# Kernel tuning notes

Measured on AMD Instinct MI355X. Metric: run time of the kernel, lower is better.

The kernel has to match this reference:

```python
import jax, jax.numpy as jnp
import numpy as np

N = 40000
E = 200000
D = 32
NUM_BANDS = 3
ORDER = 4
EPS = 1e-8
LN_EPS = 1e-5


def setup_inputs() -> dict:
    key = jax.random.key(0)
    ks = jax.random.split(key, 20)
    h = jax.random.normal(ks[0], (N, D), dtype=jnp.float32)
    Q = jax.random.normal(ks[1], (E, D, D), dtype=jnp.float32) / jnp.sqrt(jnp.float32(D))
    edge_index = jax.random.randint(ks[2], (2, E), 0, N, dtype=jnp.int32)
    coeffs = jnp.ones((NUM_BANDS, ORDER + 1), dtype=jnp.float32) / (ORDER + 1)
    s = 1.0 / np.sqrt(D)
    proj_W = jax.random.uniform(ks[3], (NUM_BANDS, D, D), minval=-s, maxval=s, dtype=jnp.float32)
    proj_b = jax.random.uniform(ks[4], (NUM_BANDS, D), minval=-s, maxval=s, dtype=jnp.float32)
    proj_g = jnp.ones((NUM_BANDS, D), dtype=jnp.float32)
    proj_beta = jnp.zeros((NUM_BANDS, D), dtype=jnp.float32)
    s3 = 1.0 / np.sqrt(NUM_BANDS * D)
    fus_W1 = jax.random.uniform(ks[5], (NUM_BANDS * D, D), minval=-s3, maxval=s3, dtype=jnp.float32)
    fus_b1 = jax.random.uniform(ks[6], (D,), minval=-s3, maxval=s3, dtype=jnp.float32)
    fus_g = jnp.ones((D,), dtype=jnp.float32)
    fus_beta = jnp.zeros((D,), dtype=jnp.float32)
    fus_W2 = jax.random.uniform(ks[7], (D, D), minval=-s, maxval=s, dtype=jnp.float32)
    fus_b2 = jax.random.uniform(ks[8], (D,), minval=-s, maxval=s, dtype=jnp.float32)
    return {"h": h, "Q": Q, "edge_index": edge_index, "coeffs": coeffs,
            "proj_W": proj_W, "proj_b": proj_b, "proj_g": proj_g, "proj_beta": proj_beta,
            "fus_W1": fus_W1, "fus_b1": fus_b1, "fus_g": fus_g, "fus_beta": fus_beta,
            "fus_W2": fus_W2, "fus_b2": fus_b2}


def _layer_norm(x, g, b):
    mu = x.mean(-1, keepdims=True)
    var = x.var(-1, keepdims=True)  # biased, as torch LayerNorm
    return (x - mu) / jnp.sqrt(var + LN_EPS) * g + b


def reference(h, Q, edge_index, coeffs, proj_W, proj_b, proj_g, proj_beta,
              fus_W1, fus_b1, fus_g, fus_beta, fus_W2, fus_b2):
    row, col = edge_index[0], edge_index[1]
    n = h.shape[0]
    ones_e = jnp.ones(row.shape[0], dtype=h.dtype)
    deg = (jax.ops.segment_sum(ones_e, row, num_segments=n)
           + jax.ops.segment_sum(ones_e, col, num_segments=n))  # [N]

    def matvec(x):
        # gather -> per-edge DxD bmm -> scatter_add; diag via degree
        Qh = jnp.einsum('eij,ej->ei', Q, x[col])          # [E, D]
        off = jax.ops.segment_sum(Qh, row, num_segments=n)  # [N, D]
        return deg[:, None] * x - off

    # power iteration for lambda_max (5 iters, fixed key for determinism)
    v = jax.random.normal(jax.random.key(42), h.shape, dtype=h.dtype)
    v = v / jnp.linalg.norm(v)
    lam = jnp.array(1.0, dtype=h.dtype)
    for _ in range(5):
        Lv = matvec(v)
        lam = (v * Lv).sum() / ((v * v).sum() + EPS)
        v = Lv / (jnp.linalg.norm(Lv) + EPS)
    lam = jnp.maximum(lam, 1.0)

    def L_tilde(x):
        return 2.0 / (lam + EPS) * matvec(x) - x

    bands = []
    for b_idx in range(NUM_BANDS):
        w = jax.nn.softmax(coeffs[b_idx])
        T_prev = h
        T_curr = L_tilde(h)
        res = w[0] * T_prev + w[1] * T_curr
        for k in range(2, ORDER + 1):
            T_next = 2.0 * L_tilde(T_curr) - T_prev
            res = res + w[k] * T_next
            T_prev, T_curr = T_curr, T_next
        p = jax.nn.silu(_layer_norm(res @ proj_W[b_idx] + proj_b[b_idx],
                                    proj_g[b_idx], proj_beta[b_idx]))
        bands.append(p)

    cat = jnp.concatenate(bands, axis=-1)  # [N, 3D]
    fused = jax.nn.silu(_layer_norm(cat @ fus_W1 + fus_b1, fus_g, fus_beta)) @ fus_W2 + fus_b2
    return h + fused
```

## Files before the change

kernel.cpp:

```cpp
#include <hip/hip_runtime.h>
#include <hip/hip_fp16.h>
#include <math.h>

#define NN 40000
#define EE 200000
#define DD 32
#define ND (NN * DD)
#define LNEPS 1e-5f

typedef float    fv4 __attribute__((ext_vector_type(4)));
typedef unsigned uv4 __attribute__((ext_vector_type(4)));

#define SLOT_ALPHA 48
#define SCAL_FLOATS (64 + 2048 + 64)

__device__ __forceinline__ void threefry2x32(unsigned k0, unsigned k1,
                                             unsigned x0, unsigned x1,
                                             unsigned& o0, unsigned& o1) {
  const unsigned k2 = k0 ^ k1 ^ 0x1BD11BDAu;
  unsigned v0 = x0 + k0, v1 = x1 + k1;
#define TF_ROUND(r) { v0 += v1; v1 = (v1 << (r)) | (v1 >> (32 - (r))); v1 ^= v0; }
  TF_ROUND(13) TF_ROUND(15) TF_ROUND(26) TF_ROUND(6)
  v0 += k1; v1 += k2 + 1u;
  TF_ROUND(17) TF_ROUND(29) TF_ROUND(16) TF_ROUND(24)
  v0 += k2; v1 += k0 + 2u;
  TF_ROUND(13) TF_ROUND(15) TF_ROUND(26) TF_ROUND(6)
  v0 += k0; v1 += k1 + 3u;
  TF_ROUND(17) TF_ROUND(29) TF_ROUND(16) TF_ROUND(24)
  v0 += k1; v1 += k2 + 4u;
  TF_ROUND(13) TF_ROUND(15) TF_ROUND(26) TF_ROUND(6)
  v0 += k2; v1 += k0 + 5u;
#undef TF_ROUND
  o0 = v0; o1 = v1;
}

__device__ __forceinline__ float wave64_sum(float x) {
  for (int o = 32; o > 0; o >>= 1) x += __shfl_xor(x, o, 64);
  return x;
}
__device__ __forceinline__ float g32_sum(float x) {
  for (int o = 16; o > 0; o >>= 1) x += __shfl_xor(x, o, 32);
  return x;
}

__global__ void k_deg(const int* __restrict__ ei, float* __restrict__ deg,
                      int* __restrict__ hist) {
  int e = blockIdx.x * 256 + threadIdx.x;
  if (e < EE) {
    int r = ei[e];
    atomicAdd(deg + r, 1.0f);
    atomicAdd(deg + ei[EE + e], 1.0f);
    atomicAdd(hist + r, 1);
  }
}

__global__ __launch_bounds__(1024) void k_scan(const int* __restrict__ hist,
                                               int* __restrict__ row_start,
                                               int* __restrict__ cursor) {
  __shared__ int part[1024];
  const int t = threadIdx.x;
  const int base = t * 40;
  int s = 0;
  for (int i = base; i < base + 40 && i < NN; ++i) s += hist[i];
  part[t] = s;
  __syncthreads();
  for (int off = 1; off < 1024; off <<= 1) {
    int v = (t >= off) ? part[t - off] : 0;
    __syncthreads();
    part[t] += v;
    __syncthreads();
  }
  int ex = (t == 0) ? 0 : part[t - 1];
  for (int i = base; i < base + 40 && i < NN; ++i) {
    row_start[i] = ex;
    cursor[i] = ex;
    ex += hist[i];
  }
  if (t == 0) row_start[NN] = EE;
}

__global__ void k_genv(float* __restrict__ v, float* __restrict__ vpre,
                       const float* __restrict__ deg) {
  int i = blockIdx.x * 256 + threadIdx.x;
  unsigned o0, o1;
  threefry2x32(0u, 42u, 0u, (unsigned)i, o0, o1);
  unsigned bits = o1;
  float f = __uint_as_float((bits >> 9) | 0x3f800000u) - 1.0f;
  const float lo = -0.99999994f;
  float u = fmaxf(lo, f * 2.0f + lo);
  float val = 1.41421354f * erfinvf(u);
  v[i] = val;
  if (vpre) vpre[i] = deg[i >> 5] * val;
}

__device__ __forceinline__ int clamp8(float q) {
  int v = (int)rintf(q);
  return v < -127 ? -127 : (v > 127 ? 127 : v);
}
__device__ __forceinline__ unsigned pack4v(fv4 q, float inv) {
  int q0 = clamp8(q.x * inv), q1 = clamp8(q.y * inv),
      q2 = clamp8(q.z * inv), q3 = clamp8(q.w * inv);
  return (q0 & 255) | ((q1 & 255) << 8) | ((q2 & 255) << 16) | ((q3 & 255) << 24);
}
__device__ __forceinline__ void dp4(unsigned u, fv4 xv, float& acc) {
  acc = fmaf((float)(signed char)(u),        xv.x, acc);
  acc = fmaf((float)(signed char)(u >> 8),   xv.y, acc);
  acc = fmaf((float)(signed char)(u >> 16),  xv.z, acc);
  acc = fmaf((float)(signed char)(u >> 24),  xv.w, acc);
}

__global__ __launch_bounds__(256) void k_cvt_mv(const float* __restrict__ x,
                                                const float* __restrict__ Q,
                                                const int* __restrict__ ei,
                                                int* __restrict__ cursor,
                                                char* __restrict__ Qi8,
                                                __half* __restrict__ Qs,
                                                int* __restrict__ cols,
                                                float* __restrict__ out) {
  const int slot = threadIdx.x >> 5;
  const int lane = threadIdx.x & 31;
  const int e = blockIdx.x * 8 + slot;
  const int row = ei[e];
  const int col = ei[EE + e];
  int pos = 0;
  if (lane == 0) pos = atomicAdd(cursor + row, 1);
  pos = __shfl(pos, 0, 32);
  const fv4* __restrict__ x4 = (const fv4*)(x + (size_t)col * DD);
  fv4 xr[8];
#pragma unroll
  for (int k = 0; k < 8; ++k) xr[k] = x4[k];
  const fv4* __restrict__ q4 =
      (const fv4*)(Q + (size_t)e * (DD * DD) + (size_t)lane * DD);
  fv4 qf[8];
#pragma unroll
  for (int k = 0; k < 8; ++k) qf[k] = __builtin_nontemporal_load(q4 + k);
  float acc = 0.0f;
#pragma unroll
  for (int k = 0; k < 8; ++k) {
    acc = fmaf(qf[k].x, xr[k].x, acc);
    acc = fmaf(qf[k].y, xr[k].y, acc);
    acc = fmaf(qf[k].z, xr[k].z, acc);
    acc = fmaf(qf[k].w, xr[k].w, acc);
  }
  float m = 0.0f;
#pragma unroll
  for (int k = 0; k < 8; ++k) {
    m = fmaxf(m, fmaxf(fmaxf(fabsf(qf[k].x), fabsf(qf[k].y)),
                       fmaxf(fabsf(qf[k].z), fabsf(qf[k].w))));
  }
  __half sh = __float2half(m * (1.0f / 127.0f));
  float s = __half2float(sh);
  float inv = (s > 0.0f) ? 1.0f / s : 0.0f;
  uv4 pa, pb;
  pa.x = pack4v(qf[0], inv); pa.y = pack4v(qf[1], inv);
  pa.z = pack4v(qf[2], inv); pa.w = pack4v(qf[3], inv);
  pb.x = pack4v(qf[4], inv); pb.y = pack4v(qf[5], inv);
  pb.z = pack4v(qf[6], inv); pb.w = pack4v(qf[7], inv);
  uv4* __restrict__ qs = (uv4*)(Qi8 + (size_t)pos * (DD * DD) + (size_t)lane * DD);
  qs[0] = pa;
  qs[1] = pb;
  Qs[pos * DD + lane] = sh;
  if (lane == 0) cols[pos] = col;
  atomicAdd(out + (size_t)row * DD + lane, -acc);
}

#define CHUNK 16

__global__ __launch_bounds__(256) void k_gather(const float* __restrict__ x,
                                                const float* __restrict__ xprev,
                                                const char* __restrict__ Qi8,
                                                const __half* __restrict__ Qs,
                                                const int* __restrict__ cols,
                                                const int* __restrict__ row_start,
                                                const float* __restrict__ deg,
                                                const float* __restrict__ scal,
                                                float* __restrict__ dots,
                                                float* __restrict__ out, int mode) {
  __shared__ float lds[4][CHUNK][DD];
  __shared__ float d1[4], d2[4];
  const int wid  = threadIdx.x >> 6;
  const int lane = threadIdx.x & 63;
  const int half = lane >> 5;
  const int d    = lane & 31;
  const int r = blockIdx.x * 4 + wid;
  const int beg = row_start[r];
  const int end = row_start[r + 1];
  const int degree = end - beg;

  const size_t idx = (size_t)r * DD + d;
  const float xi = x[idx];
  const float dv = deg[r];
  const float xp = (mode == 2) ? xprev[idx] : 0.0f;

  float acc = 0.0f;
  for (int chunk = 0; chunk < degree; chunk += CHUNK) {
    const int nchunk = min(CHUNK, degree - chunk);
    int myc = (lane < nchunk) ? cols[beg + chunk + lane] : 0;
    {
      const int el = lane >> 2;
      const int pt = lane & 3;
      if (el < nchunk) {
        const int c = __shfl(myc, el, 64);
        const fv4* __restrict__ xs = (const fv4*)(x + (size_t)c * DD);
        fv4 a = xs[pt * 2];
        fv4 b = xs[pt * 2 + 1];
        fv4* __restrict__ dst = (fv4*)&lds[wid][el][pt * 8];
        dst[0] = a;
        dst[1] = b;
      }
    }
    uv4 a0 = {0,0,0,0}, b0 = {0,0,0,0}, a1 = {0,0,0,0}, b1 = {0,0,0,0};
    float s0 = 0.0f, s1 = 0.0f;
#define LOADQ(PP, A, B, S)                                                    \
    if ((PP) < nchunk) {                                                      \
      const size_t pos = (size_t)(beg + chunk + (PP));                        \
      const uv4* __restrict__ q8 =                                            \
          (const uv4*)(Qi8 + pos * (DD * DD) + (size_t)d * DD);               \
      A = q8[0]; B = q8[1];                                                   \
      S = __half2float(Qs[pos * DD + d]);                                     \
    }
    LOADQ(half, a0, b0, s0)
    LOADQ(2 + half, a1, b1, s1)
    for (int p0 = 0; p0 < nchunk; p0 += 2) {
      uv4 a2 = {0,0,0,0}, b2 = {0,0,0,0};
      float s2 = 0.0f;
      LOADQ(p0 + 4 + half, a2, b2, s2)
      const int p = p0 + half;
      if (p < nchunk) {
        const fv4* __restrict__ xl = (const fv4*)&lds[wid][p][0];
        fv4 xr[8];
#pragma unroll
        for (int k = 0; k < 8; ++k) xr[k] = xl[k];
        float dot = 0.0f;
        dp4(a0.x, xr[0], dot); dp4(a0.y, xr[1], dot);
        dp4(a0.z, xr[2], dot); dp4(a0.w, xr[3], dot);
        dp4(b0.x, xr[4], dot); dp4(b0.y, xr[5], dot);
        dp4(b0.z, xr[6], dot); dp4(b0.w, xr[7], dot);
        acc = fmaf(s0, dot, acc);
      }
      a0 = a1; b0 = b1; s0 = s1;
      a1 = a2; b1 = b2; s1 = s2;
    }
#undef LOADQ
  }
  acc += __shfl_xor(acc, 32, 64);

  float o;
  if (mode == 1)      o = scal[SLOT_ALPHA] * (dv * xi - acc) - xi;
  else if (mode == 2) o = 2.0f * scal[SLOT_ALPHA] * (dv * xi - acc)
                          - 2.0f * xi - xp;
  else                o = dv * xi - acc;
  if (half == 0) out[idx] = o;

  if (mode == 3) {
    float p1 = (half == 0) ? o * xi : 0.0f;
    float p2 = (half == 0) ? xi * xi : 0.0f;
    p1 = wave64_sum(p1);
    p2 = wave64_sum(p2);
    if ((threadIdx.x & 63) == 0) { d1[wid] = p1; d2[wid] = p2; }
    __syncthreads();
    if (threadIdx.x == 0) {
      const int leaf = blockIdx.x & 31;
      atomicAdd(dots + 64 + leaf * 32, d1[0] + d1[1] + d1[2] + d1[3]);
      atomicAdd(dots + 64 + 1024 + leaf * 32, d2[0] + d2[1] + d2[2] + d2[3]);
    }
  }
}

__global__ void k_pre(const float* __restrict__ x, const float* __restrict__ xprev,
                      const float* __restrict__ deg, const float* __restrict__ scal,
                      float* __restrict__ out, int mode) {
  int i = blockIdx.x * 256 + threadIdx.x;
  float d = deg[i >> 5];
  float xi = x[i];
  if (mode == 0)       out[i] = d * xi;
  else if (mode == 1)  out[i] = scal[SLOT_ALPHA] * d * xi - xi;
  else                 out[i] = 2.0f * scal[SLOT_ALPHA] * d * xi - 2.0f * xi - xprev[i];
}

__global__ __launch_bounds__(256) void k_matvec(const float* __restrict__ x,
                                                const float* __restrict__ Q,
                                                const int* __restrict__ ei,
                                                float* __restrict__ out,
                                                const float* __restrict__ scal,
                                                int use_alpha, float smul) {
  const int slot = threadIdx.x >> 5;
  const int lane = threadIdx.x & 31;
  const int e = blockIdx.x * 8 + slot;
  const float factor = use_alpha ? scal[SLOT_ALPHA] * smul : smul;
  const int row = ei[e];
  const int col = ei[EE + e];
  const fv4* __restrict__ x4 = (const fv4*)(x + (size_t)col * DD);
  fv4 xr[8];
#pragma unroll
  for (int k = 0; k < 8; ++k) xr[k] = x4[k];
  const fv4* __restrict__ q4 =
      (const fv4*)(Q + (size_t)e * (DD * DD) + (size_t)lane * DD);
  float acc = 0.0f;
#pragma unroll
  for (int k = 0; k < 8; ++k) {
    fv4 q = q4[k];
    acc = fmaf(q.x, xr[k].x, acc);
    acc = fmaf(q.y, xr[k].y, acc);
    acc = fmaf(q.z, xr[k].z, acc);
    acc = fmaf(q.w, xr[k].w, acc);
  }
  atomicAdd(out + (size_t)row * DD + lane, -factor * acc);
}

#define DOT_BLOCKS 640
__global__ void k_dots(const float* __restrict__ u4, const float* __restrict__ u5,
                       float* __restrict__ scal) {
  float s1 = 0.0f, s2 = 0.0f;
  for (int i = blockIdx.x * 256 + threadIdx.x; i < ND; i += DOT_BLOCKS * 256) {
    float a = u4[i], b = u5[i];
    s1 = fmaf(a, b, s1);
    s2 = fmaf(a, a, s2);
  }
  s1 = wave64_sum(s1);
  s2 = wave64_sum(s2);
  __shared__ float ls1[4], ls2[4];
  int w = threadIdx.x >> 6;
  if ((threadIdx.x & 63) == 0) { ls1[w] = s1; ls2[w] = s2; }
  __syncthreads();
  if (threadIdx.x == 0) {
    atomicAdd(scal + 64, ls1[0] + ls1[1] + ls1[2] + ls1[3]);
    atomicAdd(scal + 64 + 1024, ls2[0] + ls2[1] + ls2[2] + ls2[3]);
  }
}

__global__ void k_alpha(float* __restrict__ scal) {
  float S1 = 0.0f, S2 = 0.0f;
  for (int l = 0; l < 32; ++l) {
    S1 += scal[64 + l * 32];
    S2 += scal[64 + 1024 + l * 32];
  }
  float lam = S1 / S2 / (1.0f + 1e-8f);
  lam = fmaxf(lam, 1.0f);
  scal[SLOT_ALPHA] = 2.0f / (lam + 1e-8f);
}

__global__ __launch_bounds__(256) void k_fuse(
    const float* __restrict__ h,
    const float* __restrict__ T1, const float* __restrict__ T2,
    const float* __restrict__ T3, const float* __restrict__ T4,
    const float* __restrict__ coeffs,
    const float* __restrict__ projW, const float* __restrict__ projb,
    const float* __restrict__ projg, const float* __restrict__ projbeta,
    const float* __restrict__ fusW1, const float* __restrict__ fusb1,
    const float* __restrict__ fusg, const float* __restrict__ fusbeta,
    const float* __restrict__ fusW2, const float* __restrict__ fusb2,
    float* __restrict__ out) {
  __shared__ float s_res[8][3][DD];
  __shared__ float s_p[8][3 * DD];
  __shared__ float s_s[8][DD];
  const int slot = threadIdx.x >> 5;
  const int lane = threadIdx.x & 31;
  const int n = blockIdx.x * 8 + slot;

  float w[3][5];
#pragma unroll
  for (int b = 0; b < 3; ++b) {
    float m = -1e30f;
#pragma unroll
    for (int k = 0; k < 5; ++k) m = fmaxf(m, coeffs[b * 5 + k]);
    float s = 0.0f;
#pragma unroll
    for (int k = 0; k < 5; ++k) { w[b][k] = expf(coeffs[b * 5 + k] - m); s += w[b][k]; }
#pragma unroll
    for (int k = 0; k < 5; ++k) w[b][k] /= s;
  }

  const int idx = n * DD + lane;
  float hd = h[idx], t1 = T1[idx], t2 = T2[idx], t3 = T3[idx], t4 = T4[idx];
#pragma unroll
  for (int b = 0; b < 3; ++b)
    s_res[slot][b][lane] =
        w[b][0] * hd + w[b][1] * t1 + w[b][2] * t2 + w[b][3] * t3 + w[b][4] * t4;
  __syncthreads();

#pragma unroll
  for (int b = 0; b < 3; ++b) {
    float y = projb[b * DD + lane];
#pragma unroll
    for (int j = 0; j < DD; ++j)
      y = fmaf(s_res[slot][b][j], projW[(b * DD + j) * DD + lane], y);
    float mu = g32_sum(y) * (1.0f / DD);
    float d = y - mu;
    float var = g32_sum(d * d) * (1.0f / DD);
    float z = d * rsqrtf(var + LNEPS) * projg[b * DD + lane] + projbeta[b * DD + lane];
    float pb = z / (1.0f + expf(-z));
    s_p[slot][b * DD + lane] = pb;
  }
  __syncthreads();

  float y = fusb1[lane];
#pragma unroll
  for (int j = 0; j < 3 * DD; ++j)
    y = fmaf(s_p[slot][j], fusW1[j * DD + lane], y);
  float mu = g32_sum(y) * (1.0f / DD);
  float d = y - mu;
  float var = g32_sum(d * d) * (1.0f / DD);
  float z = d * rsqrtf(var + LNEPS) * fusg[lane] + fusbeta[lane];
  float sv = z / (1.0f + expf(-z));
  s_s[slot][lane] = sv;
  __syncthreads();

  float o = fusb2[lane];
#pragma unroll
  for (int j = 0; j < DD; ++j)
    o = fmaf(s_s[slot][j], fusW2[j * DD + lane], o);
  out[idx] = hd + o;
}

extern "C" void kernel_launch(void* const* d_in, const int* in_sizes, int n_in,
                              void* d_out, int out_size, void* d_ws, size_t ws_size,
                              hipStream_t stream) {
  (void)in_sizes; (void)n_in; (void)out_size;
  const float* h        = (const float*)d_in[0];
  const float* Q        = (const float*)d_in[1];
  const int*   ei       = (const int*)d_in[2];
  const float* coeffs   = (const float*)d_in[3];
  const float* projW    = (const float*)d_in[4];
  const float* projb    = (const float*)d_in[5];
  const float* projg    = (const float*)d_in[6];
  const float* projbeta = (const float*)d_in[7];
  const float* fusW1    = (const float*)d_in[8];
  const float* fusb1    = (const float*)d_in[9];
  const float* fusg     = (const float*)d_in[10];
  const float* fusbeta  = (const float*)d_in[11];
  const float* fusW2    = (const float*)d_in[12];
  const float* fusb2    = (const float*)d_in[13];
  float* out = (float*)d_out;

  const size_t qi_bytes  = (size_t)EE * DD * DD;
  const size_t qs_bytes  = (size_t)EE * DD * sizeof(__half);
  const size_t col_bytes = (size_t)EE * sizeof(int);
  const size_t idx_bytes = (size_t)(2 * NN + 2) * sizeof(int);
  const size_t f32_elems = 6u * (size_t)ND + 2u * NN + SCAL_FLOATS;
  const size_t meta = qi_bytes + qs_bytes + col_bytes + idx_bytes;
  const size_t need = meta + f32_elems * sizeof(float) + 512;
  const bool fast = ws_size >= need;

  char*   Qi8 = (char*)d_ws;
  __half* Qs  = (__half*)((char*)d_ws + qi_bytes);
  int*  cols      = (int*)((char*)d_ws + qi_bytes + qs_bytes);
  int*  row_start = cols + EE;
  int*  cursor    = row_start + NN + 1;
  float* base = fast
      ? (float*)((char*)d_ws + ((meta + 255) & ~(size_t)255))
      : (float*)d_ws;
  float* uA   = base;
  float* uB   = uA + ND;
  float* T1   = uB + ND;
  float* T2   = T1 + ND;
  float* T3   = T2 + ND;
  float* T4   = T3 + ND;
  float* deg  = T4 + ND;
  float* scal = deg + NN;
  int*   hist = (int*)(scal + SCAL_FLOATS);

  (void)hipMemsetAsync(deg, 0, (2 * (size_t)NN + SCAL_FLOATS) * sizeof(float),
                       stream);

  k_deg<<<(EE + 255) / 256, 256, 0, stream>>>(ei, deg, hist);

  if (fast) {
    k_genv<<<ND / 256, 256, 0, stream>>>(uA, uB, deg);
    k_scan<<<1, 1024, 0, stream>>>(hist, row_start, cursor);
    k_cvt_mv<<<EE / 8, 256, 0, stream>>>(uA, Q, ei, cursor, Qi8, Qs, cols, uB);

    k_gather<<<NN / 4, 256, 0, stream>>>(uB, nullptr, Qi8, Qs, cols,
                                         row_start, deg, scal, scal, uA, 0);
    k_gather<<<NN / 4, 256, 0, stream>>>(uA, nullptr, Qi8, Qs, cols,
                                         row_start, deg, scal, scal, uB, 0);
    k_gather<<<NN / 4, 256, 0, stream>>>(uB, nullptr, Qi8, Qs, cols,
                                         row_start, deg, scal, scal, uA, 0);
    k_gather<<<NN / 4, 256, 0, stream>>>(uA, nullptr, Qi8, Qs, cols,
                                         row_start, deg, scal, scal, uB, 3);
    k_alpha<<<1, 1, 0, stream>>>(scal);

    const float* xin[4]   = {h, T1, T2, T3};
    const float* prevs[4] = {h, h, T1, T2};
    float* touts[4]       = {T1, T2, T3, T4};
    for (int k = 0; k < 4; ++k) {
      k_gather<<<NN / 4, 256, 0, stream>>>(xin[k], prevs[k], Qi8, Qs, cols,
                                           row_start, deg, scal, scal, touts[k],
                                           k == 0 ? 1 : 2);
    }
  } else {
    k_genv<<<ND / 256, 256, 0, stream>>>(uA, nullptr, deg);
    float* cur = uA;
    float* nxt = uB;
    for (int it = 0; it < 5; ++it) {
      k_pre<<<ND / 256, 256, 0, stream>>>(cur, nullptr, deg, scal, nxt, 0);
      k_matvec<<<EE / 8, 256, 0, stream>>>(cur, Q, ei, nxt, scal, 0, 1.0f);
      float* t = cur; cur = nxt; nxt = t;
    }
    k_dots<<<DOT_BLOCKS, 256, 0, stream>>>(nxt, cur, scal);
    k_alpha<<<1, 1, 0, stream>>>(scal);
    const float* xin[4]   = {h, T1, T2, T3};
    const float* prevs[4] = {nullptr, h, T1, T2};
    float* touts[4]       = {T1, T2, T3, T4};
    for (int k = 0; k < 4; ++k) {
      k_pre<<<ND / 256, 256, 0, stream>>>(xin[k], prevs[k], deg, scal, touts[k],
                                          k == 0 ? 1 : 2);
      k_matvec<<<EE / 8, 256, 0, stream>>>(xin[k], Q, ei, touts[k], scal, 1,
                                           k == 0 ? 1.0f : 2.0f);
    }
  }

  k_fuse<<<NN / 8, 256, 0, stream>>>(h, T1, T2, T3, T4, coeffs,
                                     projW, projb, projg, projbeta,
                                     fusW1, fusb1, fusg, fusbeta,
                                     fusW2, fusb2, out);
}
```

Baseline: 939.5 us.

## Rewrite Chebyshev recurrence in monomial basis to fuse Krylov and power-iteration passes

The Chebyshev terms are re-expressed as a monomial (Krylov) basis L^k h with precomputed conversion coefficients, so the four band matvecs no longer depend on lambda. They are launched inside the same kernels as the power-iteration matvecs, doubling the grid, and alpha powers are applied later in the fuse kernel. This removes four dependent full-graph launches, which improves concurrency and saves launch serialization. The monomial basis can be less numerically stable than the Chebyshev recurrence when powers of L grow large in magnitude.

New measurement: 911.8 us (median of 2 runs). 1.03x faster.

```diff
diff --git a/kernel.cpp b/kernel.cpp
--- a/kernel.cpp
+++ b/kernel.cpp
@@ -166,23 +166,30 @@
 
 #define CHUNK 16
 
-__global__ __launch_bounds__(256) void k_gather(const float* __restrict__ x,
-                                                const float* __restrict__ xprev,
-                                                const char* __restrict__ Qi8,
-                                                const __half* __restrict__ Qs,
-                                                const int* __restrict__ cols,
-                                                const int* __restrict__ row_start,
-                                                const float* __restrict__ deg,
-                                                const float* __restrict__ scal,
-                                                float* __restrict__ dots,
-                                                float* __restrict__ out, int mode) {
+__global__ __launch_bounds__(256) void k_gather2(const float* __restrict__ px,
+                                                 float* __restrict__ pout,
+                                                 const float* __restrict__ kxv,
+                                                 float* __restrict__ kout,
+                                                 const char* __restrict__ Qi8,
+                                                 const __half* __restrict__ Qs,
+                                                 const int* __restrict__ cols,
+                                                 const int* __restrict__ row_start,
+                                                 const float* __restrict__ deg,
+                                                 float* __restrict__ dots,
+                                                 int do_dots) {
   __shared__ float lds[4][CHUNK][DD];
   __shared__ float d1[4], d2[4];
+  const int NB = NN / 4;
+  const bool isk = blockIdx.x >= NB;
+  const int bid = isk ? blockIdx.x - NB : blockIdx.x;
+  const float* __restrict__ x = isk ? kxv : px;
+  float* __restrict__ out = isk ? kout : pout;
+
   const int wid  = threadIdx.x >> 6;
   const int lane = threadIdx.x & 63;
   const int half = lane >> 5;
   const int d    = lane & 31;
-  const int r = blockIdx.x * 4 + wid;
+  const int r = bid * 4 + wid;
   const int beg = row_start[r];
   const int end = row_start[r + 1];
   const int degree = end - beg;
@@ -190,7 +197,6 @@
   const size_t idx = (size_t)r * DD + d;
   const float xi = x[idx];
   const float dv = deg[r];
-  const float xp = (mode == 2) ? xprev[idx] : 0.0f;
 
   float acc = 0.0f;
   for (int chunk = 0; chunk < degree; chunk += CHUNK) {
@@ -245,14 +251,10 @@
   }
   acc += __shfl_xor(acc, 32, 64);
 
-  float o;
-  if (mode == 1)      o = scal[SLOT_ALPHA] * (dv * xi - acc) - xi;
-  else if (mode == 2) o = 2.0f * scal[SLOT_ALPHA] * (dv * xi - acc)
-                          - 2.0f * xi - xp;
-  else                o = dv * xi - acc;
+  const float o = dv * xi - acc;
   if (half == 0) out[idx] = o;
 
-  if (mode == 3) {
+  if (!isk && do_dots) {
     float p1 = (half == 0) ? o * xi : 0.0f;
     float p2 = (half == 0) ? xi * xi : 0.0f;
     p1 = wave64_sum(p1);
@@ -260,34 +262,26 @@
     if ((threadIdx.x & 63) == 0) { d1[wid] = p1; d2[wid] = p2; }
     __syncthreads();
     if (threadIdx.x == 0) {
-      const int leaf = blockIdx.x & 31;
+      const int leaf = bid & 31;
       atomicAdd(dots + 64 + leaf * 32, d1[0] + d1[1] + d1[2] + d1[3]);
       atomicAdd(dots + 64 + 1024 + leaf * 32, d2[0] + d2[1] + d2[2] + d2[3]);
     }
   }
 }
 
-__global__ void k_pre(const float* __restrict__ x, const float* __restrict__ xprev,
-                      const float* __restrict__ deg, const float* __restrict__ scal,
-                      float* __restrict__ out, int mode) {
+__global__ void k_pre(const float* __restrict__ x, const float* __restrict__ deg,
+                      float* __restrict__ out) {
   int i = blockIdx.x * 256 + threadIdx.x;
-  float d = deg[i >> 5];
-  float xi = x[i];
-  if (mode == 0)       out[i] = d * xi;
-  else if (mode == 1)  out[i] = scal[SLOT_ALPHA] * d * xi - xi;
-  else                 out[i] = 2.0f * scal[SLOT_ALPHA] * d * xi - 2.0f * xi - xprev[i];
+  out[i] = deg[i >> 5] * x[i];
 }
 
 __global__ __launch_bounds__(256) void k_matvec(const float* __restrict__ x,
                                                 const float* __restrict__ Q,
                                                 const int* __restrict__ ei,
-                                                float* __restrict__ out,
-                                                const float* __restrict__ scal,
-                                                int use_alpha, float smul) {
+                                                float* __restrict__ out) {
   const int slot = threadIdx.x >> 5;
   const int lane = threadIdx.x & 31;
   const int e = blockIdx.x * 8 + slot;
-  const float factor = use_alpha ? scal[SLOT_ALPHA] * smul : smul;
   const int row = ei[e];
   const int col = ei[EE + e];
   const fv4* __restrict__ x4 = (const fv4*)(x + (size_t)col * DD);
@@ -305,7 +299,7 @@
     acc = fmaf(q.z, xr[k].z, acc);
     acc = fmaf(q.w, xr[k].w, acc);
   }
-  atomicAdd(out + (size_t)row * DD + lane, -factor * acc);
+  atomicAdd(out + (size_t)row * DD + lane, -acc);
 }
 
 #define DOT_BLOCKS 640
@@ -342,8 +336,9 @@
 
 __global__ __launch_bounds__(256) void k_fuse(
     const float* __restrict__ h,
-    const float* __restrict__ T1, const float* __restrict__ T2,
-    const float* __restrict__ T3, const float* __restrict__ T4,
+    const float* __restrict__ W1, const float* __restrict__ W2,
+    const float* __restrict__ W3, const float* __restrict__ W4,
+    const float* __restrict__ scal,
     const float* __restrict__ coeffs,
     const float* __restrict__ projW, const float* __restrict__ projb,
     const float* __restrict__ projg, const float* __restrict__ projbeta,
@@ -371,37 +366,66 @@
     for (int k = 0; k < 5; ++k) w[b][k] /= s;
   }
 
+  const float C[5][5] = {
+      { 1.0f,   0.0f,   0.0f,   0.0f,  0.0f},
+      {-1.0f,   1.0f,   0.0f,   0.0f,  0.0f},
+      { 1.0f,  -4.0f,   2.0f,   0.0f,  0.0f},
+      {-1.0f,   9.0f, -12.0f,   4.0f,  0.0f},
+      { 1.0f, -16.0f,  40.0f, -32.0f,  8.0f}};
+  float cb[3][5];
+#pragma unroll
+  for (int b = 0; b < 3; ++b)
+#pragma unroll
+    for (int j = 0; j < 5; ++j) {
+      float c = 0.0f;
+#pragma unroll
+      for (int k = 0; k < 5; ++k) c = fmaf(w[b][k], C[k][j], c);
+      cb[b][j] = c;
+    }
+
+  const float alpha = scal[SLOT_ALPHA];
+  const float a1 = alpha, a2 = a1 * alpha, a3 = a2 * alpha, a4 = a3 * alpha;
+
   const int idx = n * DD + lane;
-  float hd = h[idx], t1 = T1[idx], t2 = T2[idx], t3 = T3[idx], t4 = T4[idx];
-#pragma unroll
-  for (int b = 0; b < 3; ++b)
-    s_res[slot][b][lane] =
-        w[b][0] * hd + w[b][1] * t1 + w[b][2] * t2 + w[b][3] * t3 + w[b][4] * t4;
+  const float hd = h[idx];
+  float y[5];
+  y[0] = hd;
+  y[1] = a1 * W1[idx];
+  y[2] = a2 * W2[idx];
+  y[3] = a3 * W3[idx];
+  y[4] = a4 * W4[idx];
+#pragma unroll
+  for (int b = 0; b < 3; ++b) {
+    float res = 0.0f;
+#pragma unroll
+    for (int j = 0; j < 5; ++j) res = fmaf(cb[b][j], y[j], res);
+    s_res[slot][b][lane] = res;
+  }
   __syncthreads();
 
 #pragma unroll
   for (int b = 0; b < 3; ++b) {
-    float y = projb[b * DD + lane];
+    float yv = projb[b * DD + lane];
 #pragma unroll
     for (int j = 0; j < DD; ++j)
-      y = fmaf(s_res[slot][b][j], projW[(b * DD + j) * DD + lane], y);
-    float mu = g32_sum(y) * (1.0f / DD);
-    float d = y - mu;
-    float var = g32_sum(d * d) * (1.0f / DD);
-    float z = d * rsqrtf(var + LNEPS) * projg[b * DD + lane] + projbeta[b * DD + lane];
+      yv = fmaf(s_res[slot][b][j], projW[(b * DD + j) * DD + lane], yv);
+    float mu = g32_sum(yv) * (1.0f / DD);
+    float dv = yv - mu;
+    float var = g32_sum(dv * dv) * (1.0f / DD);
+    float z = dv * rsqrtf(var + LNEPS) * projg[b * DD + lane] + projbeta[b * DD + lane];
     float pb = z / (1.0f + expf(-z));
     s_p[slot][b * DD + lane] = pb;
   }
   __syncthreads();
 
-  float y = fusb1[lane];
+  float yv = fusb1[lane];
 #pragma unroll
   for (int j = 0; j < 3 * DD; ++j)
-    y = fmaf(s_p[slot][j], fusW1[j * DD + lane], y);
-  float mu = g32_sum(y) * (1.0f / DD);
-  float d = y - mu;
-  float var = g32_sum(d * d) * (1.0f / DD);
-  float z = d * rsqrtf(var + LNEPS) * fusg[lane] + fusbeta[lane];
+    yv = fmaf(s_p[slot][j], fusW1[j * DD + lane], yv);
+  float mu = g32_sum(yv) * (1.0f / DD);
+  float dv = yv - mu;
+  float var = g32_sum(dv * dv) * (1.0f / DD);
+  float z = dv * rsqrtf(var + LNEPS) * fusg[lane] + fusbeta[lane];
   float sv = z / (1.0f + expf(-z));
   s_s[slot][lane] = sv;
   __syncthreads();
@@ -452,11 +476,11 @@
       : (float*)d_ws;
   float* uA   = base;
   float* uB   = uA + ND;
-  float* T1   = uB + ND;
-  float* T2   = T1 + ND;
-  float* T3   = T2 + ND;
-  float* T4   = T3 + ND;
-  float* deg  = T4 + ND;
+  float* W1   = uB + ND;
+  float* W2   = W1 + ND;
+  float* W3   = W2 + ND;
+  float* W4   = W3 + ND;
+  float* deg  = W4 + ND;
   float* scal = deg + NN;
   int*   hist = (int*)(scal + SCAL_FLOATS);
 
@@ -470,47 +494,36 @@
     k_scan<<<1, 1024, 0, stream>>>(hist, row_start, cursor);
     k_cvt_mv<<<EE / 8, 256, 0, stream>>>(uA, Q, ei, cursor, Qi8, Qs, cols, uB);
 
-    k_gather<<<NN / 4, 256, 0, stream>>>(uB, nullptr, Qi8, Qs, cols,
-                                         row_start, deg, scal, scal, uA, 0);
-    k_gather<<<NN / 4, 256, 0, stream>>>(uA, nullptr, Qi8, Qs, cols,
-                                         row_start, deg, scal, scal, uB, 0);
-    k_gather<<<NN / 4, 256, 0, stream>>>(uB, nullptr, Qi8, Qs, cols,
-                                         row_start, deg, scal, scal, uA, 0);
-    k_gather<<<NN / 4, 256, 0, stream>>>(uA, nullptr, Qi8, Qs, cols,
-                                         row_start, deg, scal, scal, uB, 3);
+    const int G2 = 2 * (NN / 4);
+    k_gather2<<<G2, 256, 0, stream>>>(uB, uA, h,  W1, Qi8, Qs, cols,
+                                      row_start, deg, scal, 0);
+    k_gather2<<<G2, 256, 0, stream>>>(uA, uB, W1, W2, Qi8, Qs, cols,
+                                      row_start, deg, scal, 0);
+    k_gather2<<<G2, 256, 0, stream>>>(uB, uA, W2, W3, Qi8, Qs, cols,
+                                      row_start, deg, scal, 0);
+    k_gather2<<<G2, 256, 0, stream>>>(uA, uB, W3, W4, Qi8, Qs, cols,
+                                      row_start, deg, scal, 1);
     k_alpha<<<1, 1, 0, stream>>>(scal);
-
-    const float* xin[4]   = {h, T1, T2, T3};
-    const float* prevs[4] = {h, h, T1, T2};
-    float* touts[4]       = {T1, T2, T3, T4};
-    for (int k = 0; k < 4; ++k) {
-      k_gather<<<NN / 4, 256, 0, stream>>>(xin[k], prevs[k], Qi8, Qs, cols,
-                                           row_start, deg, scal, scal, touts[k],
-                                           k == 0 ? 1 : 2);
-    }
   } else {
     k_genv<<<ND / 256, 256, 0, stream>>>(uA, nullptr, deg);
     float* cur = uA;
     float* nxt = uB;
     for (int it = 0; it < 5; ++it) {
-      k_pre<<<ND / 256, 256, 0, stream>>>(cur, nullptr, deg, scal, nxt, 0);
-      k_matvec<<<EE / 8, 256, 0, stream>>>(cur, Q, ei, nxt, scal, 0, 1.0f);
+      k_pre<<<ND / 256, 256, 0, stream>>>(cur, deg, nxt);
+      k_matvec<<<EE / 8, 256, 0, stream>>>(cur, Q, ei, nxt);
       float* t = cur; cur = nxt; nxt = t;
     }
     k_dots<<<DOT_BLOCKS, 256, 0, stream>>>(nxt, cur, scal);
     k_alpha<<<1, 1, 0, stream>>>(scal);
-    const float* xin[4]   = {h, T1, T2, T3};
-    const float* prevs[4] = {nullptr, h, T1, T2};
-    float* touts[4]       = {T1, T2, T3, T4};
+    const float* xin[4] = {h, W1, W2, W3};
+    float* wout[4]      = {W1, W2, W3, W4};
     for (int k = 0; k < 4; ++k) {
-      k_pre<<<ND / 256, 256, 0, stream>>>(xin[k], prevs[k], deg, scal, touts[k],
-                                          k == 0 ? 1 : 2);
-      k_matvec<<<EE / 8, 256, 0, stream>>>(xin[k], Q, ei, touts[k], scal, 1,
-                                           k == 0 ? 1.0f : 2.0f);
-    }
-  }
-
-  k_fuse<<<NN / 8, 256, 0, stream>>>(h, T1, T2, T3, T4, coeffs,
+      k_pre<<<ND / 256, 256, 0, stream>>>(xin[k], deg, wout[k]);
+      k_matvec<<<EE / 8, 256, 0, stream>>>(xin[k], Q, ei, wout[k]);
+    }
+  }
+
+  k_fuse<<<NN / 8, 256, 0, stream>>>(h, W1, W2, W3, W4, scal, coeffs,
                                      projW, projb, projg, projbeta,
                                      fusW1, fusb1, fusg, fusbeta,
                                      fusW2, fusb2, out);
```
